# Kernel optimization log

Measured on AMD Instinct MI355X. Metric: run time of the kernel, lower is better.

## Reference

```python
import jax, jax.numpy as jnp
import numpy as np

NUM_CONN = 8

def _ein_reduce(f):
    # Einstein t-norm fold over last axis: T(a,b) = ab / (2 - (a+b-ab))
    acc = f[..., 0]
    for i in range(1, f.shape[-1]):
        b = f[..., i]
        ab = acc * b
        acc = ab / (2.0 - (acc + b - ab))
    return acc

def _coein_reduce(f):
    # Einstein t-conorm fold over last axis: S(a,b) = (a+b) / (1 + ab)
    acc = f[..., 0]
    for i in range(1, f.shape[-1]):
        b = f[..., i]
        acc = (acc + b) / (1.0 + acc * b)
    return acc

def _ddlg_layer(x, w, idx, is_train):
    # x: [B, in], idx: [out, C] int, w: [out, 4]
    feats = x[:, idx]                      # [B, out, C] gather
    ops = jnp.stack([
        jnp.min(feats, axis=-1),
        jnp.max(feats, axis=-1),
        _ein_reduce(feats),
        _coein_reduce(feats),
    ], axis=-1)                            # [B, out, 4]
    if is_train:
        prob = jax.nn.softmax(w, axis=-1)  # [out, 4]
    else:
        prob = jax.nn.one_hot(jnp.argmax(w, axis=-1), 4, dtype=x.dtype)
    return jnp.einsum('bof,of->bo', ops, prob)

def setup_inputs() -> dict:
    key = jax.random.key(0)
    ks = jax.random.split(key, 6)
    sizes = [4096, 2048, 1024, 2048, 4096]
    x = jax.random.uniform(ks[0], (4096, sizes[0]), dtype=jnp.float32)
    ws = [jax.random.normal(ks[1 + i], (sizes[i + 1], 4), dtype=jnp.float32) for i in range(4)]
    rng = np.random.default_rng(0)
    idxs = []
    for i in range(4):
        # randperm-without-replacement per output neuron
        perm = np.argsort(rng.random((sizes[i + 1], sizes[i])), axis=-1)[:, :NUM_CONN]
        idxs.append(jnp.asarray(perm, dtype=jnp.int32))
    return {
        'x': x,
        'w0': ws[0], 'w1': ws[1], 'w2': ws[2], 'w3': ws[3],
        'idx0': idxs[0], 'idx1': idxs[1], 'idx2': idxs[2], 'idx3': idxs[3],
        'is_train': 1,
    }

def reference(x, w0, w1, w2, w3, idx0, idx1, idx2, idx3, is_train):
    h = _ddlg_layer(x, w0, idx0, is_train)
    h = _ddlg_layer(h, w1, idx1, is_train)
    h = _ddlg_layer(h, w2, idx2, is_train)
    h = _ddlg_layer(h, w3, idx3, is_train)
    return h
```

## Files before the change

kernel.cpp:

```cpp
#include <hip/hip_runtime.h>
#include <hip/hip_bf16.h>


#define BATCH 4096

typedef _Float16 h4 __attribute__((ext_vector_type(4)));

__device__ __forceinline__ float fastrcp(float x) { return __builtin_amdgcn_rcpf(x); }
__device__ __forceinline__ _Float16 hrcp(_Float16 x) {
#if __has_builtin(__builtin_amdgcn_rcph)
    return __builtin_amdgcn_rcph(x);
#else
    return (_Float16)__builtin_amdgcn_rcpf((float)x);
#endif
}
__device__ __forceinline__ h4 splat(_Float16 s) { h4 v = {s, s, s, s}; return v; }

__global__ __launch_bounds__(256) void prep_k(const float* __restrict__ w0,
                                              const float* __restrict__ w1,
                                              const float* __restrict__ w2,
                                              const float* __restrict__ w3,
                                              const int* __restrict__ is_train,
                                              const int4* __restrict__ idx0,
                                              const int4* __restrict__ idx1,
                                              const int4* __restrict__ idx2,
                                              const int4* __restrict__ idx3,
                                              h4* __restrict__ probsH,
                                              int4* __restrict__ idxS) {
    const int blk = blockIdx.x;
    if (blk < 36) {
        int g = blk * 256 + threadIdx.x;
        if (g >= 9216) return;
        const float* w; int o;
        if (g < 2048)      { w = w0; o = g; }
        else if (g < 3072) { w = w1; o = g - 2048; }
        else if (g < 5120) { w = w2; o = g - 3072; }
        else               { w = w3; o = g - 5120; }
        float wv[4];
#pragma unroll
        for (int c = 0; c < 4; ++c) wv[c] = w[(o << 2) + c];
        float p[4];
        if (*is_train) {
            float m = fmaxf(fmaxf(wv[0], wv[1]), fmaxf(wv[2], wv[3]));
            float s = 0.0f;
#pragma unroll
            for (int c = 0; c < 4; ++c) { p[c] = __expf(wv[c] - m); s += p[c]; }
            float inv = fastrcp(s);
#pragma unroll
            for (int c = 0; c < 4; ++c) p[c] *= inv;
        } else {
            int a = 0; float best = wv[0];
#pragma unroll
            for (int c = 1; c < 4; ++c) if (wv[c] > best) { best = wv[c]; a = c; }
#pragma unroll
            for (int c = 0; c < 4; ++c) p[c] = (c == a) ? 1.0f : 0.0f;
        }
        probsH[g] = h4{(_Float16)p[0], (_Float16)p[1], (_Float16)p[2], (_Float16)p[3]};
    } else {
        int g = (blk - 36) * 256 + threadIdx.x;
        const int4* src; int off;
        if (g < 4096)       { src = idx0; off = g; }
        else if (g < 6144)  { src = idx1; off = g - 4096; }
        else if (g < 10240) { src = idx2; off = g - 6144; }
        else                { src = idx3; off = g - 10240; }
        int4 v = src[off];
        idxS[g] = int4{v.x << 2, v.y << 2, v.z << 2, v.w << 2};
    }
}

__device__ __forceinline__ h4 gate4h(const _Float16* __restrict__ src,
                                     const int4* __restrict__ idx,
                                     const h4* __restrict__ probs,
                                     int o) {
    const int4 i0 = idx[o * 2];
    const int4 i1 = idx[o * 2 + 1];
    const h4 P = probs[o];
    h4 raw[8];
    raw[0] = *(const h4*)(src + i0.x);
    raw[1] = *(const h4*)(src + i0.y);
    raw[2] = *(const h4*)(src + i0.z);
    raw[3] = *(const h4*)(src + i0.w);
    raw[4] = *(const h4*)(src + i1.x);
    raw[5] = *(const h4*)(src + i1.y);
    raw[6] = *(const h4*)(src + i1.z);
    raw[7] = *(const h4*)(src + i1.w);

    const h4 one = splat((_Float16)1.0f);
    const h4 two = splat((_Float16)2.0f);

    h4 mn = raw[0], mx = raw[0], De = raw[0];
    h4 Ne = two - raw[0];
    h4 Nc = one + raw[0];
    h4 Dc = one - raw[0];
#pragma unroll
    for (int c = 1; c < 8; ++c) {
        h4 v = raw[c];
        mn = __builtin_elementwise_min(mn, v);
        mx = __builtin_elementwise_max(mx, v);
        De *= v;
        Ne *= (two - v);
        Nc += Nc * v;
        Dc -= Dc * v;
    }
    h4 s1 = Ne + De;
    h4 s2 = Nc + Dc;
    h4 d1 = Nc - Dc;
    h4 r1, r2;
#pragma unroll
    for (int e = 0; e < 4; ++e) { r1[e] = hrcp(s1[e]); r2[e] = hrcp(s2[e]); }
    h4 ein = (De + De) * r1;
    h4 coe = d1 * r2;
    h4 res = splat(P[0]) * mn;
    res += splat(P[1]) * mx;
    res += splat(P[2]) * ein;
    res += splat(P[3]) * coe;
    return res;
}

__device__ __forceinline__ void layer_pass(const _Float16* __restrict__ src,
                                           _Float16* __restrict__ dst,
                                           const int4* __restrict__ idx,
                                           const h4* __restrict__ probs,
                                           int o) {
    h4 r = gate4h(src, idx, probs, o);
    *(h4*)(dst + (o << 2)) = r;
}

__global__ __launch_bounds__(1024, 8) void ddlg_fused(const float* __restrict__ x,
                                                      const h4* __restrict__ probsH,
                                                      const int4* __restrict__ idxS,
                                                      float* __restrict__ out) {
    __shared__ __align__(16) _Float16 lds[24576];
    const int t  = threadIdx.x;
    const int b0 = blockIdx.x << 2;

    const _Float16* xl = lds;
    _Float16*       h0 = lds + 16384;
    _Float16*       h1 = lds;
    _Float16*       h2 = lds + 16384;

#pragma unroll
    for (int c = 0; c < 4; ++c) {
        const int j = (c << 10) + t;
        const float v0 = x[(size_t)(b0 + 0) * 4096 + j];
        const float v1 = x[(size_t)(b0 + 1) * 4096 + j];
        const float v2 = x[(size_t)(b0 + 2) * 4096 + j];
        const float v3 = x[(size_t)(b0 + 3) * 4096 + j];
        h4 hv;
        hv[0] = (_Float16)v0; hv[1] = (_Float16)v1;
        hv[2] = (_Float16)v2; hv[3] = (_Float16)v3;
        *(h4*)(lds + (j << 2)) = hv;
    }
    __syncthreads();

    layer_pass(xl, h0, idxS, probsH, t);
    layer_pass(xl, h0, idxS, probsH, t + 1024);
    __syncthreads();

    layer_pass(h0, h1, idxS + 4096, probsH + 2048, t);
    __syncthreads();

    layer_pass(h1, h2, idxS + 6144, probsH + 3072, t);
    layer_pass(h1, h2, idxS + 6144, probsH + 3072, t + 1024);
    __syncthreads();

#pragma unroll
    for (int p = 0; p < 4; ++p) {
        const int o = (p << 10) + t;
        h4 r = gate4h(h2, idxS + 10240, probsH + 5120, o);
#pragma unroll
        for (int b = 0; b < 4; ++b)
            out[(size_t)(b0 + b) * 4096 + o] = (float)r[b];
    }
}

extern "C" void kernel_launch(void* const* d_in, const int* in_sizes, int n_in,
                              void* d_out, int out_size, void* d_ws, size_t ws_size,
                              hipStream_t stream) {
    const float* x        = (const float*)d_in[0];
    const float* w0       = (const float*)d_in[1];
    const float* w1       = (const float*)d_in[2];
    const float* w2       = (const float*)d_in[3];
    const float* w3       = (const float*)d_in[4];
    const int4*  idx0     = (const int4*)d_in[5];
    const int4*  idx1     = (const int4*)d_in[6];
    const int4*  idx2     = (const int4*)d_in[7];
    const int4*  idx3     = (const int4*)d_in[8];
    const int*   is_train = (const int*)d_in[9];
    float*       out      = (float*)d_out;

    h4*   probsH = (h4*)d_ws;
    int4* idxS   = (int4*)((char*)d_ws + (128 << 10));

    prep_k<<<108, 256, 0, stream>>>(w0, w1, w2, w3, is_train,
                                    idx0, idx1, idx2, idx3, probsH, idxS);
    ddlg_fused<<<1024, 1024, 0, stream>>>(x, probsH, idxS, out);
}
```

Baseline: 165.7 us.

## Prefetch next layer's indices and probs during compute; drop index pre-scaling

```diff
diff --git a/kernel.cpp b/kernel.cpp
--- a/kernel.cpp
+++ b/kernel.cpp
@@ -1,5 +1,4 @@
 #include <hip/hip_runtime.h>
-#include <hip/hip_bf16.h>
 
 
 #define BATCH 4096
@@ -21,69 +20,56 @@
                                               const float* __restrict__ w2,
                                               const float* __restrict__ w3,
                                               const int* __restrict__ is_train,
-                                              const int4* __restrict__ idx0,
-                                              const int4* __restrict__ idx1,
-                                              const int4* __restrict__ idx2,
-                                              const int4* __restrict__ idx3,
-                                              h4* __restrict__ probsH,
-                                              int4* __restrict__ idxS) {
-    const int blk = blockIdx.x;
-    if (blk < 36) {
-        int g = blk * 256 + threadIdx.x;
-        if (g >= 9216) return;
-        const float* w; int o;
-        if (g < 2048)      { w = w0; o = g; }
-        else if (g < 3072) { w = w1; o = g - 2048; }
-        else if (g < 5120) { w = w2; o = g - 3072; }
-        else               { w = w3; o = g - 5120; }
-        float wv[4];
-#pragma unroll
-        for (int c = 0; c < 4; ++c) wv[c] = w[(o << 2) + c];
-        float p[4];
-        if (*is_train) {
-            float m = fmaxf(fmaxf(wv[0], wv[1]), fmaxf(wv[2], wv[3]));
-            float s = 0.0f;
-#pragma unroll
-            for (int c = 0; c < 4; ++c) { p[c] = __expf(wv[c] - m); s += p[c]; }
-            float inv = fastrcp(s);
-#pragma unroll
-            for (int c = 0; c < 4; ++c) p[c] *= inv;
-        } else {
-            int a = 0; float best = wv[0];
-#pragma unroll
-            for (int c = 1; c < 4; ++c) if (wv[c] > best) { best = wv[c]; a = c; }
-#pragma unroll
-            for (int c = 0; c < 4; ++c) p[c] = (c == a) ? 1.0f : 0.0f;
-        }
-        probsH[g] = h4{(_Float16)p[0], (_Float16)p[1], (_Float16)p[2], (_Float16)p[3]};
+                                              h4* __restrict__ probsH) {
+    const int g = blockIdx.x * 256 + threadIdx.x;
+    const float* w; int o;
+    if (g < 2048)      { w = w0; o = g; }
+    else if (g < 3072) { w = w1; o = g - 2048; }
+    else if (g < 5120) { w = w2; o = g - 3072; }
+    else               { w = w3; o = g - 5120; }
+    float wv[4];
+#pragma unroll
+    for (int c = 0; c < 4; ++c) wv[c] = w[(o << 2) + c];
+    float p[4];
+    if (*is_train) {
+        float m = fmaxf(fmaxf(wv[0], wv[1]), fmaxf(wv[2], wv[3]));
+        float s = 0.0f;
+#pragma unroll
+        for (int c = 0; c < 4; ++c) { p[c] = __expf(wv[c] - m); s += p[c]; }
+        float inv = fastrcp(s);
+#pragma unroll
+        for (int c = 0; c < 4; ++c) p[c] *= inv;
     } else {
-        int g = (blk - 36) * 256 + threadIdx.x;
-        const int4* src; int off;
-        if (g < 4096)       { src = idx0; off = g; }
-        else if (g < 6144)  { src = idx1; off = g - 4096; }
-        else if (g < 10240) { src = idx2; off = g - 6144; }
-        else                { src = idx3; off = g - 10240; }
-        int4 v = src[off];
-        idxS[g] = int4{v.x << 2, v.y << 2, v.z << 2, v.w << 2};
-    }
-}
-
-__device__ __forceinline__ h4 gate4h(const _Float16* __restrict__ src,
-                                     const int4* __restrict__ idx,
-                                     const h4* __restrict__ probs,
-                                     int o) {
-    const int4 i0 = idx[o * 2];
-    const int4 i1 = idx[o * 2 + 1];
-    const h4 P = probs[o];
+        int a = 0; float best = wv[0];
+#pragma unroll
+        for (int c = 1; c < 4; ++c) if (wv[c] > best) { best = wv[c]; a = c; }
+#pragma unroll
+        for (int c = 0; c < 4; ++c) p[c] = (c == a) ? 1.0f : 0.0f;
+    }
+    probsH[g] = h4{(_Float16)p[0], (_Float16)p[1], (_Float16)p[2], (_Float16)p[3]};
+}
+
+struct GatePre { int4 i0, i1; h4 P; };
+
+__device__ __forceinline__ GatePre pre_load(const int4* __restrict__ idx,
+                                            const h4* __restrict__ probs, int o) {
+    GatePre g;
+    g.i0 = idx[o * 2];
+    g.i1 = idx[o * 2 + 1];
+    g.P  = probs[o];
+    return g;
+}
+
+__device__ __forceinline__ h4 gate_body(const h4* __restrict__ rows, const GatePre g) {
     h4 raw[8];
-    raw[0] = *(const h4*)(src + i0.x);
-    raw[1] = *(const h4*)(src + i0.y);
-    raw[2] = *(const h4*)(src + i0.z);
-    raw[3] = *(const h4*)(src + i0.w);
-    raw[4] = *(const h4*)(src + i1.x);
-    raw[5] = *(const h4*)(src + i1.y);
-    raw[6] = *(const h4*)(src + i1.z);
-    raw[7] = *(const h4*)(src + i1.w);
+    raw[0] = rows[g.i0.x];
+    raw[1] = rows[g.i0.y];
+    raw[2] = rows[g.i0.z];
+    raw[3] = rows[g.i0.w];
+    raw[4] = rows[g.i1.x];
+    raw[5] = rows[g.i1.y];
+    raw[6] = rows[g.i1.z];
+    raw[7] = rows[g.i1.w];
 
     const h4 one = splat((_Float16)1.0f);
     const h4 two = splat((_Float16)2.0f);
@@ -110,34 +96,31 @@
     for (int e = 0; e < 4; ++e) { r1[e] = hrcp(s1[e]); r2[e] = hrcp(s2[e]); }
     h4 ein = (De + De) * r1;
     h4 coe = d1 * r2;
-    h4 res = splat(P[0]) * mn;
-    res += splat(P[1]) * mx;
-    res += splat(P[2]) * ein;
-    res += splat(P[3]) * coe;
+    h4 res = splat(g.P[0]) * mn;
+    res += splat(g.P[1]) * mx;
+    res += splat(g.P[2]) * ein;
+    res += splat(g.P[3]) * coe;
     return res;
-}
-
-__device__ __forceinline__ void layer_pass(const _Float16* __restrict__ src,
-                                           _Float16* __restrict__ dst,
-                                           const int4* __restrict__ idx,
-                                           const h4* __restrict__ probs,
-                                           int o) {
-    h4 r = gate4h(src, idx, probs, o);
-    *(h4*)(dst + (o << 2)) = r;
 }
 
 __global__ __launch_bounds__(1024, 8) void ddlg_fused(const float* __restrict__ x,
                                                       const h4* __restrict__ probsH,
-                                                      const int4* __restrict__ idxS,
+                                                      const int4* __restrict__ idx0,
+                                                      const int4* __restrict__ idx1,
+                                                      const int4* __restrict__ idx2,
+                                                      const int4* __restrict__ idx3,
                                                       float* __restrict__ out) {
     __shared__ __align__(16) _Float16 lds[24576];
     const int t  = threadIdx.x;
     const int b0 = blockIdx.x << 2;
 
-    const _Float16* xl = lds;
-    _Float16*       h0 = lds + 16384;
-    _Float16*       h1 = lds;
-    _Float16*       h2 = lds + 16384;
+    const h4* xl = (const h4*)lds;
+    const h4* h0 = (const h4*)(lds + 16384);
+    const h4* h1 = (const h4*)lds;
+    const h4* h2 = (const h4*)(lds + 16384);
+
+    GatePre gA = pre_load(idx0, probsH, t);
+    GatePre gB = pre_load(idx0, probsH, t + 1024);
 
 #pragma unroll
     for (int c = 0; c < 4; ++c) {
@@ -153,24 +136,55 @@
     }
     __syncthreads();
 
-    layer_pass(xl, h0, idxS, probsH, t);
-    layer_pass(xl, h0, idxS, probsH, t + 1024);
-    __syncthreads();
-
-    layer_pass(h0, h1, idxS + 4096, probsH + 2048, t);
-    __syncthreads();
-
-    layer_pass(h1, h2, idxS + 6144, probsH + 3072, t);
-    layer_pass(h1, h2, idxS + 6144, probsH + 3072, t + 1024);
-    __syncthreads();
-
-#pragma unroll
-    for (int p = 0; p < 4; ++p) {
-        const int o = (p << 10) + t;
-        h4 r = gate4h(h2, idxS + 10240, probsH + 5120, o);
-#pragma unroll
-        for (int b = 0; b < 4; ++b)
-            out[(size_t)(b0 + b) * 4096 + o] = (float)r[b];
+    {
+        h4 r = gate_body(xl, gA);
+        gA = pre_load(idx1, probsH + 2048, t);
+        *(h4*)(lds + 16384 + (t << 2)) = r;
+        r = gate_body(xl, gB);
+        gB = pre_load(idx2, probsH + 3072, t);
+        *(h4*)(lds + 16384 + ((t + 1024) << 2)) = r;
+    }
+    __syncthreads();
+
+    {
+        h4 r = gate_body(h0, gA);
+        gA = pre_load(idx2, probsH + 3072, t + 1024);
+        *(h4*)(lds + (t << 2)) = r;
+    }
+    __syncthreads();
+
+    {
+        h4 r = gate_body(h1, gB);
+        gB = pre_load(idx3, probsH + 5120, t);
+        *(h4*)(lds + 16384 + (t << 2)) = r;
+        r = gate_body(h1, gA);
+        gA = pre_load(idx3, probsH + 5120, t + 1024);
+        *(h4*)(lds + 16384 + ((t + 1024) << 2)) = r;
+    }
+    __syncthreads();
+
+    {
+        h4 r = gate_body(h2, gB);
+        gB = pre_load(idx3, probsH + 5120, t + 2048);
+#pragma unroll
+        for (int b = 0; b < 4; ++b)
+            out[(size_t)(b0 + b) * 4096 + t] = (float)r[b];
+
+        r = gate_body(h2, gA);
+        gA = pre_load(idx3, probsH + 5120, t + 3072);
+#pragma unroll
+        for (int b = 0; b < 4; ++b)
+            out[(size_t)(b0 + b) * 4096 + (t + 1024)] = (float)r[b];
+
+        r = gate_body(h2, gB);
+#pragma unroll
+        for (int b = 0; b < 4; ++b)
+            out[(size_t)(b0 + b) * 4096 + (t + 2048)] = (float)r[b];
+
+        r = gate_body(h2, gA);
+#pragma unroll
+        for (int b = 0; b < 4; ++b)
+            out[(size_t)(b0 + b) * 4096 + (t + 3072)] = (float)r[b];
     }
 }
 
@@ -189,10 +203,8 @@
     const int*   is_train = (const int*)d_in[9];
     float*       out      = (float*)d_out;
 
-    h4*   probsH = (h4*)d_ws;
-    int4* idxS   = (int4*)((char*)d_ws + (128 << 10));
-
-    prep_k<<<108, 256, 0, stream>>>(w0, w1, w2, w3, is_train,
-                                    idx0, idx1, idx2, idx3, probsH, idxS);
-    ddlg_fused<<<1024, 1024, 0, stream>>>(x, probsH, idxS, out);
-}
+    h4* probsH = (h4*)d_ws;
+
+    prep_k<<<36, 256, 0, stream>>>(w0, w1, w2, w3, is_train, probsH);
+    ddlg_fused<<<1024, 1024, 0, stream>>>(x, probsH, idx0, idx1, idx2, idx3, out);
+}
```

Result: no change. 165.1 us (-0.4%).
